# Optimization experiments

Measured on AMD Instinct MI355X. Metric: run time of the kernel, lower is better.

## Reference

```python
import jax, jax.numpy as jnp
import numpy as np

HEAD_SIZE = 128
D_MODEL = 1024


def setup_inputs() -> dict:
    key = jax.random.key(0)
    kx, kq, kk, kv = jax.random.split(key, 4)
    B, T, C = 8, 2048, D_MODEL
    scale = 1.0 / np.sqrt(C)
    x = jax.random.normal(kx, (B, T, C), dtype=jnp.float32)
    # Dense(head_size, use_bias=False) weights, shape [C, head_size]
    Wq = jax.random.normal(kq, (C, HEAD_SIZE), dtype=jnp.float32) * scale
    Wk = jax.random.normal(kk, (C, HEAD_SIZE), dtype=jnp.float32) * scale
    Wv = jax.random.normal(kv, (C, HEAD_SIZE), dtype=jnp.float32) * scale
    return {"x": x, "Wq": Wq, "Wk": Wk, "Wv": Wv}


def reference(x, Wq, Wk, Wv):
    B, T, C = x.shape
    q = jnp.einsum('btc,ch->bth', x, Wq)  # [B,T,H]
    k = jnp.einsum('btc,ch->bth', x, Wk)
    v = jnp.einsum('btc,ch->bth', x, Wv)
    # NOTE: original scales by C**-0.5 (input channels), not head_size**-0.5
    scale = jnp.asarray(C, x.dtype) ** -0.5
    wei = jnp.einsum('bqh,bkh->bqk', q, k) * scale  # [B,T,T]
    causal = jnp.tril(jnp.ones((T, T), dtype=bool))
    wei = jnp.where(causal, wei, -jnp.inf)
    wei = jax.nn.softmax(wei, axis=-1)
    # dropout is identity in inference mode
    out = jnp.einsum('bqk,bkh->bqh', wei, v)  # [B,T,H]
    return out
```

## Files before the change

kernel.cpp:

```cpp
#include <hip/hip_runtime.h>

#define HS 128
#define DM 1024
#define BB 8
#define TT 2048

typedef __bf16 bf16;
typedef __bf16 bf16x8 __attribute__((ext_vector_type(8)));
typedef float f32x4 __attribute__((ext_vector_type(4)));

#define MFMA16(a, b, c) __builtin_amdgcn_mfma_f32_16x16x32_bf16(a, b, c, 0, 0, 0)
#define RAW_BARRIER() asm volatile("s_barrier" ::: "memory")

__device__ __forceinline__ void gll16(const bf16* g, bf16* l) {
  __builtin_amdgcn_global_load_lds(
      (const __attribute__((address_space(1))) void*)g,
      (__attribute__((address_space(3))) void*)l, 16, 0, 0);
}
__device__ __forceinline__ void gll16f(const float* g, float* l) {
  __builtin_amdgcn_global_load_lds(
      (const __attribute__((address_space(1))) void*)g,
      (__attribute__((address_space(3))) void*)l, 16, 0, 0);
}

__global__ __launch_bounds__(256) void wt_kernel(const float* __restrict__ Wq,
                                                 const float* __restrict__ Wk,
                                                 const float* __restrict__ Wv,
                                                 bf16* __restrict__ Wt) {
  __shared__ bf16 lt[128][72];
  const int mat = blockIdx.y;
  const float* W = mat == 0 ? Wq : (mat == 1 ? Wk : Wv);
  const int k0 = blockIdx.x * 64;
  const int t = threadIdx.x;
  for (int i = 0; i < 32; ++i) {
    int idx = t + i * 256;
    int k = idx >> 7;
    int h = idx & 127;
    lt[h][k] = (bf16)W[(size_t)(k0 + k) * HS + h];
  }
  __syncthreads();
  int h = t >> 1, half = t & 1;
  const uint4* src = (const uint4*)&lt[h][half * 32];
  uint4* dst = (uint4*)(Wt + ((size_t)mat * 128 + h) * DM + k0 + half * 32);
  dst[0] = src[0]; dst[1] = src[1]; dst[2] = src[2]; dst[3] = src[3];
}

__global__ __launch_bounds__(512) void qkv_kernel(const float* __restrict__ x,
                                                  const bf16* __restrict__ Wt,
                                                  bf16* __restrict__ Q,
                                                  bf16* __restrict__ K,
                                                  bf16* __restrict__ Vt) {
  __shared__ __align__(16) char qsm[114688];
  float (*xsf)[8192] = (float(*)[8192])qsm;
  bf16 (*wsb)[12288] = (bf16(*)[12288])(qsm + 65536);
  bf16* vts = (bf16*)qsm;
  const int t = threadIdx.x, w = t >> 6, lane = t & 63, rl = lane & 15, quad = lane >> 4;
  const int rt = blockIdx.x >> 1, nb = blockIdx.x & 1;
  const int row0 = rt * 128;
  const int rw = w & 3, cw = w >> 2;
  f32x4 acc[2][6] = {};

  auto stage = [&](int kt, int bufi) {
#pragma unroll
    for (int i2 = 0; i2 < 4; ++i2) {
      int s = w * 4 + i2;
      int row = s * 4 + (lane >> 4);
      int cg = (lane & 15) ^ (row & 15);
      gll16f(x + (size_t)(row0 + row) * DM + kt * 64 + cg * 4, &xsf[bufi][s * 256]);
    }
#pragma unroll
    for (int i2 = 0; i2 < 3; ++i2) {
      int s = w * 3 + i2;
      int row = s * 8 + (lane >> 3);
      int cg = (lane & 7) ^ (row & 7);
      gll16(Wt + (size_t)(nb * 192 + row) * DM + kt * 64 + cg * 8, &wsb[bufi][s * 512]);
    }
  };

  stage(0, 0);
  stage(1, 1);
  for (int kt = 0; kt < 16; ++kt) {
    const int cur = kt & 1;
    if (kt < 15) asm volatile("s_waitcnt vmcnt(7)" ::: "memory");
    else         asm volatile("s_waitcnt vmcnt(0)" ::: "memory");
    RAW_BARRIER();
#pragma unroll
    for (int kc = 0; kc < 2; ++kc) {
      bf16x8 a[2];
#pragma unroll
      for (int rf = 0; rf < 2; ++rf) {
        int ar = rw * 32 + rf * 16 + rl;
        int c0 = kc * 8 + quad * 2;
        float4 f0 = *(const float4*)&xsf[cur][ar * 64 + (((c0) ^ (ar & 15)) << 2)];
        float4 f1 = *(const float4*)&xsf[cur][ar * 64 + (((c0 + 1) ^ (ar & 15)) << 2)];
        bf16x8 tv;
        tv[0] = (bf16)f0.x; tv[1] = (bf16)f0.y; tv[2] = (bf16)f0.z; tv[3] = (bf16)f0.w;
        tv[4] = (bf16)f1.x; tv[5] = (bf16)f1.y; tv[6] = (bf16)f1.z; tv[7] = (bf16)f1.w;
        a[rf] = tv;
      }
#pragma unroll
      for (int cf = 0; cf < 6; ++cf) {
        int br = cw * 96 + cf * 16 + rl;
        int cb = kc * 4 + quad;
        bf16x8 bb = *(const bf16x8*)&wsb[cur][br * 64 + ((cb ^ (br & 7)) << 3)];
        acc[0][cf] = MFMA16(a[0], bb, acc[0][cf]);
        acc[1][cf] = MFMA16(a[1], bb, acc[1][cf]);
      }
    }
    RAW_BARRIER();
    if (kt < 14) stage(kt + 2, cur);
  }
#pragma unroll
  for (int cf = 0; cf < 6; ++cf) {
    int cg = nb * 192 + cw * 96 + cf * 16 + rl;
    int mat = cg >> 7, hcol = cg & 127;
    if (mat < 2) {
      bf16* dst = mat == 0 ? Q : K;
#pragma unroll
      for (int rf = 0; rf < 2; ++rf)
#pragma unroll
        for (int r = 0; r < 4; ++r) {
          int tg = row0 + rw * 32 + rf * 16 + quad * 4 + r;
          dst[((size_t)tg << 7) + hcol] = (bf16)acc[rf][cf][r];
        }
    } else {
#pragma unroll
      for (int rf = 0; rf < 2; ++rf)
#pragma unroll
        for (int r = 0; r < 4; ++r) {
          int trow = rw * 32 + rf * 16 + quad * 4 + r;
          vts[hcol * 136 + trow] = (bf16)acc[rf][cf][r];
        }
    }
  }
  if (nb == 1) {
    __syncthreads();
    const int h = t >> 2, q4 = t & 3;
    const bf16* src = vts + h * 136 + q4 * 32;
    bf16* dst = Vt + ((size_t)((row0 >> 11) * 128 + h) << 11) + (row0 & 2047) + q4 * 32;
#pragma unroll
    for (int j = 0; j < 4; ++j)
      ((bf16x8*)dst)[j] = ((const bf16x8*)src)[j];
  }
}

__global__ __launch_bounds__(256) void attn_kernel(const bf16* __restrict__ Qb,
                                                   const bf16* __restrict__ Kb,
                                                   const bf16* __restrict__ Vtb,
                                                   float* __restrict__ out) {
  __shared__ __align__(16) char smem[79104];
  bf16* qs = (bf16*)smem;
  bf16* ks = (bf16*)(smem + 8192);
  bf16* vt = (bf16*)(smem + 40960);
  float* Of = (float*)smem;
  float* ml = (float*)(smem + 78848);
  const int t = threadIdx.x, w = t >> 6, lane = t & 63, rl = lane & 15, quad = lane >> 4;
  const int wrow = w >> 1, kh = w & 1;
  const int rank = blockIdx.x >> 3, b = blockIdx.x & 7;
  const int qi = 63 - rank;
  const int q0 = qi * 32;
  const size_t base = (size_t)b * TT;
  const int KT = (qi >> 1) + 1;

#pragma unroll
  for (int i2 = 0; i2 < 2; ++i2) {
    int s = w * 2 + i2;
    int row = s * 4 + (lane >> 4);
    int ch = (lane & 15) ^ (row & 15);
    gll16(Qb + ((base + q0 + row) << 7) + ch * 8, qs + s * 512);
  }
  auto stageKV = [&](int slot) {
    int kt = min(slot, KT - 1);
    int bufi = slot & 1;
    bf16* ksb = ks + bufi * 8192;
    bf16* vtb = vt + bufi * 8192;
#pragma unroll
    for (int i2 = 0; i2 < 4; ++i2) {
      int s = w * 4 + i2;
      int rowk = s * 4 + (lane >> 4);
      int chk = (lane & 15) ^ (rowk & 15);
      gll16(Kb + ((base + kt * 64 + rowk) << 7) + chk * 8, ksb + s * 512);
      int rowv = s * 8 + (lane >> 3);
      int chv = (lane & 7) ^ (rowv & 7);
      gll16(Vtb + ((size_t)(b * 128 + rowv) << 11) + kt * 64 + chv * 8, vtb + s * 512);
    }
  };
  stageKV(0);
  stageKV(1);

  f32x4 o[8] = {};
  float lrow[4] = {0.f, 0.f, 0.f, 0.f};
  bf16x8 aq[4];
  bf16* psw = (bf16*)(smem + 73728) + w * 640;

  for (int i = 0; i < KT; ++i) {
    const int cur = i & 1;
    asm volatile("s_waitcnt vmcnt(8)" ::: "memory");
    RAW_BARRIER();
    if (i == 0) {
      const int arow = wrow * 16 + rl;
#pragma unroll
      for (int hc = 0; hc < 4; ++hc)
        aq[hc] = *(const bf16x8*)(qs + arow * 128 + ((((hc << 2) + quad) ^ (arow & 15)) << 3));
    }
    bf16* ksb = ks + cur * 8192;
    bf16* vtb = vt + cur * 8192;
    f32x4 s4[2] = {};
#pragma unroll
    for (int hc = 0; hc < 4; ++hc) {
#pragma unroll
      for (int c = 0; c < 2; ++c) {
        int brow = (kh * 2 + c) * 16 + rl;
        bf16x8 bb = *(const bf16x8*)(ksb + brow * 128 + ((((hc << 2) + quad) ^ (brow & 15)) << 3));
        s4[c] = MFMA16(aq[hc], bb, s4[c]);
      }
    }
    const bool diag = (i == KT - 1);
#pragma unroll
    for (int r = 0; r < 4; ++r) {
      int rloc = quad * 4 + r;
      int rowg = q0 + wrow * 16 + rloc;
      float psum = 0.f;
#pragma unroll
      for (int c = 0; c < 2; ++c) {
        int colg = i * 64 + kh * 32 + c * 16 + rl;
        float p = (diag && colg > rowg) ? 0.f : __expf(s4[c][r] * 0.03125f - 6.0f);
        psum += p;
        psw[rloc * 40 + c * 16 + rl] = (bf16)p;
      }
      lrow[r] += psum;
    }
    bf16x8 pa = *(const bf16x8*)(psw + rl * 40 + quad * 8);
#pragma unroll
    for (int ht = 0; ht < 8; ++ht) {
      int brow = ht * 16 + rl;
      bf16x8 bb = *(const bf16x8*)(vtb + brow * 64 + ((((kh << 2) + quad) ^ (brow & 7)) << 3));
      o[ht] = MFMA16(pa, bb, o[ht]);
    }
    RAW_BARRIER();
    if (i + 2 <= KT) stageKV(i + 2);
  }

#pragma unroll
  for (int r = 0; r < 4; ++r)
#pragma unroll
    for (int off = 1; off < 16; off <<= 1) lrow[r] += __shfl_xor(lrow[r], off, 64);
  __syncthreads();
#pragma unroll
  for (int ht = 0; ht < 8; ++ht)
#pragma unroll
    for (int r = 0; r < 4; ++r)
      Of[kh * 4096 + (wrow * 16 + quad * 4 + r) * 128 + ht * 16 + rl] = o[ht][r];
  if (rl == 0)
#pragma unroll
    for (int r = 0; r < 4; ++r) ml[kh * 32 + wrow * 16 + quad * 4 + r] = lrow[r];
  __syncthreads();
#pragma unroll
  for (int r = 0; r < 4; ++r) {
    int rowl = wrow * 16 + quad * 4 + r;
    float inv = 1.f / (ml[rowl] + ml[32 + rowl]);
#pragma unroll
    for (int hh = 0; hh < 4; ++hh) {
      int col = kh * 64 + hh * 16 + rl;
      out[((base + q0 + rowl) << 7) + col] =
          (Of[rowl * 128 + col] + Of[4096 + rowl * 128 + col]) * inv;
    }
  }
}

extern "C" void kernel_launch(void* const* d_in, const int* in_sizes, int n_in,
                              void* d_out, int out_size, void* d_ws, size_t ws_size,
                              hipStream_t stream) {
  const float* x = (const float*)d_in[0];
  const float* Wq = (const float*)d_in[1];
  const float* Wk = (const float*)d_in[2];
  const float* Wv = (const float*)d_in[3];
  float* out = (float*)d_out;
  char* ws = (char*)d_ws;
  bf16* Wt = (bf16*)ws;
  bf16* Q = (bf16*)(ws + 786432);
  bf16* K = (bf16*)(ws + 786432 + 4194304);
  bf16* Vt = (bf16*)(ws + 786432 + 2 * 4194304);
  wt_kernel<<<dim3(16, 3), 256, 0, stream>>>(Wq, Wk, Wv, Wt);
  qkv_kernel<<<dim3(256), 512, 0, stream>>>(x, Wt, Q, K, Vt);
  attn_kernel<<<dim3(512), 256, 0, stream>>>(Q, K, Vt, out);
}
```

Measured before the change: 159.5 us.

## Convert x to bf16 via registers and triple-buffer QKV projection pipeline

The QKV projection kernel now loads fp32 x tiles into registers, converts them to bf16 once, and writes them to swizzled LDS. Previously fp32 went straight to LDS and was converted on every fragment read. Weight tiles move to a three-buffer ring with finer-grained waits, barriers and setprio around the MFMA bursts, and the warp tiling changes from 4x2 to 2x4 (4x3 fragments per wave). The aim is less LDS traffic and conversion work in the inner loop and more overlap of global loads with MFMA. The cost is more registers for the prefetched x and a fragile hand-tuned vmcnt schedule.

```diff
diff --git a/kernel.cpp b/kernel.cpp
--- a/kernel.cpp
+++ b/kernel.cpp
@@ -13,11 +13,6 @@
 #define RAW_BARRIER() asm volatile("s_barrier" ::: "memory")
 
 __device__ __forceinline__ void gll16(const bf16* g, bf16* l) {
-  __builtin_amdgcn_global_load_lds(
-      (const __attribute__((address_space(1))) void*)g,
-      (__attribute__((address_space(3))) void*)l, 16, 0, 0);
-}
-__device__ __forceinline__ void gll16f(const float* g, float* l) {
   __builtin_amdgcn_global_load_lds(
       (const __attribute__((address_space(1))) void*)g,
       (__attribute__((address_space(3))) void*)l, 16, 0, 0);
@@ -50,85 +45,135 @@
                                                   bf16* __restrict__ Q,
                                                   bf16* __restrict__ K,
                                                   bf16* __restrict__ Vt) {
-  __shared__ __align__(16) char qsm[114688];
-  float (*xsf)[8192] = (float(*)[8192])qsm;
-  bf16 (*wsb)[12288] = (bf16(*)[12288])(qsm + 65536);
+  __shared__ __align__(16) char qsm[122880];
+  bf16* xls = (bf16*)qsm;
+  bf16* wls = (bf16*)(qsm + 49152);
   bf16* vts = (bf16*)qsm;
   const int t = threadIdx.x, w = t >> 6, lane = t & 63, rl = lane & 15, quad = lane >> 4;
   const int rt = blockIdx.x >> 1, nb = blockIdx.x & 1;
   const int row0 = rt * 128;
-  const int rw = w & 3, cw = w >> 2;
-  f32x4 acc[2][6] = {};
-
-  auto stage = [&](int kt, int bufi) {
-#pragma unroll
-    for (int i2 = 0; i2 < 4; ++i2) {
-      int s = w * 4 + i2;
-      int row = s * 4 + (lane >> 4);
-      int cg = (lane & 15) ^ (row & 15);
-      gll16f(x + (size_t)(row0 + row) * DM + kt * 64 + cg * 4, &xsf[bufi][s * 256]);
-    }
+  const int rw = w & 1, cw = w >> 1;
+  f32x4 acc[4][3] = {};
+  float4 xra[4], xrb[4];
+
+  const int xrow = w * 16 + rl;
+  const int xkc = quad;
+
+  auto stageW = [&](int j, int bufi) {
+    bf16* dst = wls + bufi * 12288;
 #pragma unroll
     for (int i2 = 0; i2 < 3; ++i2) {
       int s = w * 3 + i2;
       int row = s * 8 + (lane >> 3);
       int cg = (lane & 7) ^ (row & 7);
-      gll16(Wt + (size_t)(nb * 192 + row) * DM + kt * 64 + cg * 8, &wsb[bufi][s * 512]);
-    }
-  };
-
-  stage(0, 0);
-  stage(1, 1);
-  for (int kt = 0; kt < 16; ++kt) {
-    const int cur = kt & 1;
-    if (kt < 15) asm volatile("s_waitcnt vmcnt(7)" ::: "memory");
-    else         asm volatile("s_waitcnt vmcnt(0)" ::: "memory");
-    RAW_BARRIER();
-#pragma unroll
-    for (int kc = 0; kc < 2; ++kc) {
-      bf16x8 a[2];
-#pragma unroll
-      for (int rf = 0; rf < 2; ++rf) {
-        int ar = rw * 32 + rf * 16 + rl;
-        int c0 = kc * 8 + quad * 2;
-        float4 f0 = *(const float4*)&xsf[cur][ar * 64 + (((c0) ^ (ar & 15)) << 2)];
-        float4 f1 = *(const float4*)&xsf[cur][ar * 64 + (((c0 + 1) ^ (ar & 15)) << 2)];
-        bf16x8 tv;
-        tv[0] = (bf16)f0.x; tv[1] = (bf16)f0.y; tv[2] = (bf16)f0.z; tv[3] = (bf16)f0.w;
-        tv[4] = (bf16)f1.x; tv[5] = (bf16)f1.y; tv[6] = (bf16)f1.z; tv[7] = (bf16)f1.w;
-        a[rf] = tv;
-      }
-#pragma unroll
-      for (int cf = 0; cf < 6; ++cf) {
-        int br = cw * 96 + cf * 16 + rl;
-        int cb = kc * 4 + quad;
-        bf16x8 bb = *(const bf16x8*)&wsb[cur][br * 64 + ((cb ^ (br & 7)) << 3)];
-        acc[0][cf] = MFMA16(a[0], bb, acc[0][cf]);
-        acc[1][cf] = MFMA16(a[1], bb, acc[1][cf]);
-      }
-    }
-    RAW_BARRIER();
-    if (kt < 14) stage(kt + 2, cur);
-  }
-#pragma unroll
-  for (int cf = 0; cf < 6; ++cf) {
-    int cg = nb * 192 + cw * 96 + cf * 16 + rl;
+      gll16(Wt + (size_t)(nb * 192 + row) * DM + j * 64 + cg * 8, dst + s * 512);
+    }
+  };
+  auto loadX = [&](int j, float4 (&xr)[4]) {
+    const float* p = x + (size_t)(row0 + xrow) * DM + j * 64 + xkc * 16;
+#pragma unroll
+    for (int i = 0; i < 4; ++i) xr[i] = *(const float4*)(p + i * 4);
+  };
+  auto writeX = [&](int bufi, float4 (&xr)[4]) {
+    bf16* dst = xls + bufi * 8192 + xrow * 64;
+#pragma unroll
+    for (int hh = 0; hh < 2; ++hh) {
+      float4 a0 = xr[hh * 2], a1 = xr[hh * 2 + 1];
+      bf16x8 tv;
+      tv[0] = (bf16)a0.x; tv[1] = (bf16)a0.y; tv[2] = (bf16)a0.z; tv[3] = (bf16)a0.w;
+      tv[4] = (bf16)a1.x; tv[5] = (bf16)a1.y; tv[6] = (bf16)a1.z; tv[7] = (bf16)a1.w;
+      int L = xkc * 2 + hh;
+      *(bf16x8*)(dst + ((L ^ (xrow & 7)) << 3)) = tv;
+    }
+  };
+
+  auto step = [&](int kt, float4 (&xu)[4], float4 (&xl)[4]) {
+    const int cur = kt % 3, nxt = (kt + 1) % 3, nx2 = (kt + 2) % 3;
+    const bf16* xc = xls + cur * 8192;
+    const bf16* wc = wls + cur * 12288;
+    const int j2 = (kt + 2 < 16) ? kt + 2 : 15;
+    asm volatile("s_waitcnt vmcnt(7) lgkmcnt(0)" ::: "memory");
+    RAW_BARRIER();
+    bf16x8 af[4], bf[3];
+#pragma unroll
+    for (int rf = 0; rf < 4; ++rf) {
+      int ar = rw * 64 + rf * 16 + rl;
+      af[rf] = *(const bf16x8*)(xc + ar * 64 + ((quad ^ (ar & 7)) << 3));
+    }
+#pragma unroll
+    for (int cf = 0; cf < 3; ++cf) {
+      int br = cw * 48 + cf * 16 + rl;
+      bf[cf] = *(const bf16x8*)(wc + br * 64 + ((quad ^ (br & 7)) << 3));
+    }
+    loadX(j2, xl);
+    RAW_BARRIER();
+    asm volatile("s_waitcnt lgkmcnt(0)" ::: "memory");
+    __builtin_amdgcn_sched_barrier(0);
+    __builtin_amdgcn_s_setprio(1);
+#pragma unroll
+    for (int rf = 0; rf < 4; ++rf)
+#pragma unroll
+      for (int cf = 0; cf < 3; ++cf)
+        acc[rf][cf] = MFMA16(af[rf], bf[cf], acc[rf][cf]);
+    __builtin_amdgcn_s_setprio(0);
+#pragma unroll
+    for (int rf = 0; rf < 4; ++rf) {
+      int ar = rw * 64 + rf * 16 + rl;
+      af[rf] = *(const bf16x8*)(xc + ar * 64 + (((4 + quad) ^ (ar & 7)) << 3));
+    }
+#pragma unroll
+    for (int cf = 0; cf < 3; ++cf) {
+      int br = cw * 48 + cf * 16 + rl;
+      bf[cf] = *(const bf16x8*)(wc + br * 64 + (((4 + quad) ^ (br & 7)) << 3));
+    }
+    stageW(j2, nx2);
+    RAW_BARRIER();
+    asm volatile("s_waitcnt lgkmcnt(0)" ::: "memory");
+    __builtin_amdgcn_sched_barrier(0);
+    __builtin_amdgcn_s_setprio(1);
+#pragma unroll
+    for (int rf = 0; rf < 4; ++rf)
+#pragma unroll
+      for (int cf = 0; cf < 3; ++cf)
+        acc[rf][cf] = MFMA16(af[rf], bf[cf], acc[rf][cf]);
+    __builtin_amdgcn_s_setprio(0);
+    asm volatile("s_waitcnt vmcnt(10)" ::: "memory");
+    writeX(nxt, xu);
+  };
+
+  loadX(0, xra);
+  stageW(0, 0);
+  loadX(1, xrb);
+  stageW(1, 1);
+  asm volatile("s_waitcnt vmcnt(10)" ::: "memory");
+  writeX(0, xra);
+
+  for (int kt = 0; kt < 16; kt += 2) {
+    step(kt, xrb, xra);
+    step(kt + 1, xra, xrb);
+  }
+
+  asm volatile("s_waitcnt vmcnt(0) lgkmcnt(0)" ::: "memory");
+  __syncthreads();
+#pragma unroll
+  for (int cf = 0; cf < 3; ++cf) {
+    int cg = nb * 192 + cw * 48 + cf * 16 + rl;
     int mat = cg >> 7, hcol = cg & 127;
     if (mat < 2) {
       bf16* dst = mat == 0 ? Q : K;
 #pragma unroll
-      for (int rf = 0; rf < 2; ++rf)
+      for (int rf = 0; rf < 4; ++rf)
 #pragma unroll
         for (int r = 0; r < 4; ++r) {
-          int tg = row0 + rw * 32 + rf * 16 + quad * 4 + r;
+          int tg = row0 + rw * 64 + rf * 16 + quad * 4 + r;
           dst[((size_t)tg << 7) + hcol] = (bf16)acc[rf][cf][r];
         }
     } else {
 #pragma unroll
-      for (int rf = 0; rf < 2; ++rf)
+      for (int rf = 0; rf < 4; ++rf)
 #pragma unroll
         for (int r = 0; r < 4; ++r) {
-          int trow = rw * 32 + rf * 16 + quad * 4 + r;
+          int trow = rw * 64 + rf * 16 + quad * 4 + r;
           vts[hcol * 136 + trow] = (bf16)acc[rf][cf][r];
         }
     }
```

After: 163.0 us. 2.2% more time.
